# Optimization experiments

Measured on AMD Instinct MI355X. Metric: run time of the kernel, lower is better.

Reference implementation:

```python
import jax, jax.numpy as jnp
import numpy as np

B, S, D, H = 64, 1024, 512, 512

def setup_inputs() -> dict:
    key = jax.random.key(0)
    ks = jax.random.split(key, 10)
    w = 0.04  # ~xavier scale for 512x512
    return {
        "inputs": jax.random.normal(ks[0], (B, S, D), jnp.float32),
        "Wxi": jax.random.normal(ks[1], (D, H), jnp.float32) * w,
        "Whi": jax.random.normal(ks[2], (H, H), jnp.float32) * w,
        "bi": jnp.zeros((H,), jnp.float32),
        "Wxf": jax.random.normal(ks[3], (D, H), jnp.float32) * w,
        "Whf": jax.random.normal(ks[4], (H, H), jnp.float32) * w,
        "bf": jnp.zeros((H,), jnp.float32),
        "Wxo": jax.random.normal(ks[5], (D, H), jnp.float32) * w,
        "Who": jax.random.normal(ks[6], (H, H), jnp.float32) * w,
        "bo": jnp.zeros((H,), jnp.float32),
        "Wxc": jax.random.normal(ks[7], (D, H), jnp.float32) * w,
        "Whc": jax.random.normal(ks[8], (H, H), jnp.float32) * w,
        "bc": jnp.zeros((H,), jnp.float32),
    }

def reference(inputs, Wxi, Whi, bi, Wxf, Whf, bf, Wxo, Who, bo, Wxc, Whc, bc):
    b, s, _ = inputs.shape
    h = Whi.shape[0]
    # Precompute input projections for all timesteps (same math, batched GEMM).
    xi = inputs @ Wxi + bi  # [B,S,H]
    xf = inputs @ Wxf + bf
    xo = inputs @ Wxo + bo
    xc = inputs @ Wxc + bc
    # time-major for scan: [S,B,H]
    xs = tuple(jnp.swapaxes(a, 0, 1) for a in (xi, xf, xo, xc))

    def step(carry, x_t):
        h_t, c_t = carry
        xi_t, xf_t, xo_t, xc_t = x_t
        i = jax.nn.sigmoid(xi_t + h_t @ Whi)
        f = jax.nn.sigmoid(xf_t + h_t @ Whf)
        o = jax.nn.sigmoid(xo_t + h_t @ Who)
        g = jnp.tanh(xc_t + h_t @ Whc)
        c_new = f * c_t + i * g
        h_new = o * jnp.tanh(c_new)
        return (h_new, c_new), h_new

    h0 = jnp.zeros((b, h), inputs.dtype)
    c0 = jnp.zeros((b, h), inputs.dtype)
    (h_fin, c_fin), out = jax.lax.scan(step, (h0, c0), xs)
    outputs = jnp.swapaxes(out, 0, 1)  # [B,S,H]
    h_final = h_fin[None]  # [1,B,H] (num_layers*num_directions=1)
    c_final = c_fin[None]
    return (outputs, h_final, c_final)
```

## Files before the change

kernel.cpp:

```cpp
#include <hip/hip_runtime.h>
#include <hip/hip_bf16.h>

typedef __attribute__((ext_vector_type(8))) short short8;
typedef __attribute__((ext_vector_type(4))) float f32x4;
typedef __attribute__((ext_vector_type(4))) unsigned int u32x4;

#define NB 64
#define NS 1024
#define ND 512
#define NH 512
#define NG 2048
#define M1 65536

#define OFF_A    0L
#define OFF_XG   67108864L
#define OFF_WXT  335544320L
#define OFF_WHT  337641472L
#define OFF_BC   339738624L
#define OFF_HB   339746816L
#define OFF_BAR  339877888L

#define OUT_HF   33554432L
#define OUT_CF   33587200L

#define LDS_STRIDE 264

static __device__ __forceinline__ ushort f2bf(float x) {
  union { float f; unsigned u; } v; v.f = x;
  unsigned r = (v.u + 0x7FFFu + ((v.u >> 16) & 1u)) >> 16;
  return (ushort)r;
}
static __device__ __forceinline__ float bf2f(ushort x) {
  union { unsigned u; float f; } v; v.u = ((unsigned)x) << 16; return v.f;
}
static __device__ __forceinline__ float sigm(float x) {
  return 1.0f / (1.0f + __expf(-x));
}
static __device__ __forceinline__ float tanh_fast(float x) {
  return 2.0f / (1.0f + __expf(-2.0f * x)) - 1.0f;
}

__global__ __launch_bounds__(256) void cvt_in_k(const float* __restrict__ in,
                                                ushort* __restrict__ out) {
  long i = ((long)blockIdx.x * 256 + threadIdx.x) * 8;
  const float4* p = (const float4*)(in + i);
  float4 a = p[0], b = p[1];
  short8 o;
  o[0] = (short)f2bf(a.x); o[1] = (short)f2bf(a.y);
  o[2] = (short)f2bf(a.z); o[3] = (short)f2bf(a.w);
  o[4] = (short)f2bf(b.x); o[5] = (short)f2bf(b.y);
  o[6] = (short)f2bf(b.z); o[7] = (short)f2bf(b.w);
  *(short8*)(out + i) = o;
}

__global__ __launch_bounds__(256) void prep_w_k(
    const float* __restrict__ Wxi, const float* __restrict__ Whi, const float* __restrict__ bi,
    const float* __restrict__ Wxf, const float* __restrict__ Whf, const float* __restrict__ bff,
    const float* __restrict__ Wxo, const float* __restrict__ Who, const float* __restrict__ bo,
    const float* __restrict__ Wxc, const float* __restrict__ Whc, const float* __restrict__ bc,
    ushort* __restrict__ Wxt, ushort* __restrict__ Wht, float* __restrict__ bcat) {
  int t = blockIdx.x * 256 + threadIdx.x;
  int n = t >> 9, k = t & 511;
  int g = n >> 9, col = n & 511;
  const float* wx = (g == 0) ? Wxi : (g == 1) ? Wxf : (g == 2) ? Wxo : Wxc;
  const float* wh = (g == 0) ? Whi : (g == 1) ? Whf : (g == 2) ? Who : Whc;
  Wxt[t] = f2bf(wx[k * 512 + col]);
  Wht[t] = f2bf(wh[k * 512 + col]);
  if (t < 2048) {
    int g2 = t >> 9;
    const float* bp = (g2 == 0) ? bi : (g2 == 1) ? bff : (g2 == 2) ? bo : bc;
    bcat[t] = bp[t & 511];
  }
}

__global__ __launch_bounds__(256) void gemm_x_k(const ushort* __restrict__ A,
                                                const ushort* __restrict__ Bt,
                                                const float* __restrict__ bcat,
                                                ushort* __restrict__ xg) {
  __shared__ ushort As[128 * 40];
  __shared__ ushort Bs[128 * 40];
  const int mbase = blockIdx.x * 128;
  const int nbase = blockIdx.y * 128;
  const int tid = threadIdx.x;
  const int lane = tid & 63, wave = tid >> 6;
  const int l15 = lane & 15, q = lane >> 4;
  const int wm = (wave & 1) * 64, wn = (wave >> 1) * 64;

  f32x4 acc[4][4];
#pragma unroll
  for (int j = 0; j < 4; ++j) {
    float bv = bcat[nbase + wn + j * 16 + l15];
#pragma unroll
    for (int i = 0; i < 4; ++i) acc[i][j] = (f32x4){bv, bv, bv, bv};
  }

  const int sr = tid >> 2;
  const int skk = (tid & 3) * 8;

  for (int kt = 0; kt < 16; ++kt) {
    const int kb = kt * 32;
#pragma unroll
    for (int pass = 0; pass < 2; ++pass) {
      int rr = sr + pass * 64;
      *(short8*)&As[rr * 40 + skk] = *(const short8*)&A[(long)(mbase + rr) * 512 + kb + skk];
      *(short8*)&Bs[rr * 40 + skk] = *(const short8*)&Bt[(long)(nbase + rr) * 512 + kb + skk];
    }
    __syncthreads();
    short8 af[4], bfr[4];
#pragma unroll
    for (int i = 0; i < 4; ++i)
      af[i] = *(const short8*)&As[(wm + i * 16 + l15) * 40 + q * 8];
#pragma unroll
    for (int j = 0; j < 4; ++j)
      bfr[j] = *(const short8*)&Bs[(wn + j * 16 + l15) * 40 + q * 8];
#pragma unroll
    for (int i = 0; i < 4; ++i)
#pragma unroll
      for (int j = 0; j < 4; ++j)
        acc[i][j] = __builtin_amdgcn_mfma_f32_16x16x32_bf16(af[i], bfr[j], acc[i][j], 0, 0, 0);
    __syncthreads();
  }

#pragma unroll
  for (int i = 0; i < 4; ++i) {
#pragma unroll
    for (int r = 0; r < 4; ++r) {
      int m = mbase + wm + i * 16 + q * 4 + r;
      int b = m >> 10, s = m & 1023;
      long rowoff = ((long)(s * 64 + b)) * 2048;
#pragma unroll
      for (int j = 0; j < 4; ++j) {
        int n = nbase + wn + j * 16 + l15;
        xg[rowoff + n] = f2bf(acc[i][j][r]);
      }
    }
  }
}

__global__ __launch_bounds__(256, 1) void lstm_rec_k(const ushort* __restrict__ xg,
                                                     const ushort* __restrict__ Wht,
                                                     float* __restrict__ out,
                                                     unsigned* hb, unsigned* ctrl) {
  const int wg = blockIdx.x;
  const int g = wg & 7, r = wg >> 3;
  const int tid = threadIdx.x;
  const int wave = tid >> 6, lane = tid & 63;
  const int l15 = lane & 15, q = lane >> 4;

  __shared__ unsigned hs[8 * LDS_STRIDE];

  unsigned* fl  = ctrl + g * 32;
  unsigned* hbg = hb + g * 4096;
  const ushort* xgg = xg + (long)g * 8 * 2048;

  short8 bfrag[2][16];
  int gcol[2];
#pragma unroll
  for (int p = 0; p < 2; ++p) {
    int nloc = p * 16 + l15;
    gcol[p] = (nloc >> 3) * 512 + r * 32 + wave * 8 + (nloc & 7);
#pragma unroll
    for (int kt = 0; kt < 16; ++kt)
      bfrag[p][kt] = *(const short8*)&Wht[(long)gcol[p] * 512 + kt * 32 + q * 8];
  }
#pragma unroll
  for (int p = 0; p < 2; ++p)
#pragma unroll
    for (int kt = 0; kt < 16; ++kt)
      asm volatile("" : "+v"(bfrag[p][kt]));

  float xpre[2][4] = {{0.f, 0.f, 0.f, 0.f}, {0.f, 0.f, 0.f, 0.f}};
  if (q < 2) {
#pragma unroll
    for (int p = 0; p < 2; ++p)
#pragma unroll
      for (int rr = 0; rr < 4; ++rr)
        xpre[p][rr] = bf2f(xgg[(long)(q * 4 + rr) * 2048 + gcol[p]]);
  }

  const bool wr = (lane & 8) == 0;
  const bool wrp = wr && ((lane & 1) == 0);
  float c4[4] = {0.f, 0.f, 0.f, 0.f};
  float hsave[4] = {0.f, 0.f, 0.f, 0.f};
  float hpsave[4] = {0.f, 0.f, 0.f, 0.f};

  const int c0 = tid, c1 = tid + 256;
  const int l0 = (c0 >> 6) * LDS_STRIDE + (c0 & 63) * 4;
  const int l1 = (c1 >> 6) * LDS_STRIDE + (c1 & 63) * 4;

  for (int t = 0; t < 1024; ++t) {
    union { unsigned long long u[2]; short8 s8; } afu[16];

    if (t > 0) {
      const unsigned* gb = hbg + (t & 1) * 2048;
      u32x4 va, vb;
      asm volatile(
          "global_load_dwordx4 %0, %2, off sc0 sc1\n\t"
          "global_load_dwordx4 %1, %3, off sc0 sc1"
          : "=&v"(va), "=&v"(vb)
          : "v"(gb + c0 * 4), "v"(gb + c1 * 4)
          : "memory");
      asm volatile("s_waitcnt vmcnt(0)" ::: "memory");
      *(u32x4*)&hs[l0] = va;
      *(u32x4*)&hs[l1] = vb;
      __syncthreads();

      if (l15 < 8) {
        const unsigned* lb = &hs[l15 * LDS_STRIDE + q * 4];
#pragma unroll
        for (int kt = 0; kt < 16; ++kt)
          afu[kt].s8 = *(const short8*)(lb + kt * 16);
      } else {
#pragma unroll
        for (int kt = 0; kt < 16; ++kt) { afu[kt].u[0] = 0ull; afu[kt].u[1] = 0ull; }
      }
    } else {
#pragma unroll
      for (int kt = 0; kt < 16; ++kt) { afu[kt].u[0] = 0ull; afu[kt].u[1] = 0ull; }
    }

    f32x4 acc[2];
#pragma unroll
    for (int p = 0; p < 2; ++p)
#pragma unroll
      for (int rr = 0; rr < 4; ++rr)
        acc[p][rr] = xpre[p][rr];

#pragma unroll
    for (int kt = 0; kt < 16; ++kt) {
      acc[0] = __builtin_amdgcn_mfma_f32_16x16x32_bf16(afu[kt].s8, bfrag[0][kt], acc[0], 0, 0, 0);
      acc[1] = __builtin_amdgcn_mfma_f32_16x16x32_bf16(afu[kt].s8, bfrag[1][kt], acc[1], 0, 0, 0);
    }

    unsigned* hdst = hbg + ((t + 1) & 1) * 2048;
#pragma unroll
    for (int rr = 0; rr < 4; ++rr) {
      float a0 = acc[0][rr], a1 = acc[1][rr];
      float o0 = __shfl_xor(a0, 8);
      float o1 = __shfl_xor(a1, 8);
      float pi = wr ? a0 : o0;
      float pf = wr ? o0 : a0;
      float po = wr ? a1 : o1;
      float pg = wr ? o1 : a1;
      float ig = sigm(pi), fg = sigm(pf), og = sigm(po), gg = tanh_fast(pg);
      float cc = fg * c4[rr] + ig * gg;
      c4[rr] = cc;
      float hn = og * tanh_fast(cc);
      float hnp = __shfl_xor(hn, 1);
      hsave[rr] = hn;
      hpsave[rr] = hnp;
      if (wrp && q < 2 && t < 1023) {
        unsigned pack = (unsigned)f2bf(hn) | ((unsigned)f2bf(hnp) << 16);
        __hip_atomic_store(&hdst[(q * 4 + rr) * 256 + r * 16 + wave * 4 + ((lane & 6) >> 1)],
                           pack, __ATOMIC_RELAXED, __HIP_MEMORY_SCOPE_AGENT);
      }
    }

    if (t < 1023) {
      __syncthreads();
      if (tid == 0)
        __hip_atomic_store(&fl[r], (unsigned)(t + 1), __ATOMIC_RELAXED,
                           __HIP_MEMORY_SCOPE_AGENT);
    }

    if (wrp && q < 2) {
#pragma unroll
      for (int rr = 0; rr < 4; ++rr)
        *(float2*)&out[(long)(g * 8 + q * 4 + rr) * (NS * NH) + (long)t * NH +
                       r * 32 + wave * 8 + (lane & 6)] =
            make_float2(hsave[rr], hpsave[rr]);
    }

    if (t < 1023) {
      long xb2 = ((long)(t + 1) * 64) * 2048;
      if (q < 2) {
#pragma unroll
        for (int p = 0; p < 2; ++p)
#pragma unroll
          for (int rr = 0; rr < 4; ++rr)
            xpre[p][rr] = bf2f(xgg[xb2 + (long)(q * 4 + rr) * 2048 + gcol[p]]);
      }
      if (wave == 0 && lane < 16) {
        unsigned tgt = (unsigned)(t + 1);
        while (__hip_atomic_load(&fl[lane], __ATOMIC_RELAXED,
                                 __HIP_MEMORY_SCOPE_AGENT) < tgt) {}
      }
      __syncthreads();
    }
  }

  if (wr && q < 2) {
    int hcol = r * 32 + wave * 8 + (lane & 7);
#pragma unroll
    for (int rr = 0; rr < 4; ++rr) {
      int b = g * 8 + q * 4 + rr;
      out[OUT_HF + (long)b * 512 + hcol] = hsave[rr];
      out[OUT_CF + (long)b * 512 + hcol] = c4[rr];
    }
  }
}

extern "C" void kernel_launch(void* const* d_in, const int* in_sizes, int n_in,
                              void* d_out, int out_size, void* d_ws, size_t ws_size,
                              hipStream_t stream) {
  const float* inputs = (const float*)d_in[0];
  const float* Wxi = (const float*)d_in[1];
  const float* Whi = (const float*)d_in[2];
  const float* bi  = (const float*)d_in[3];
  const float* Wxf = (const float*)d_in[4];
  const float* Whf = (const float*)d_in[5];
  const float* bff = (const float*)d_in[6];
  const float* Wxo = (const float*)d_in[7];
  const float* Who = (const float*)d_in[8];
  const float* bo  = (const float*)d_in[9];
  const float* Wxc = (const float*)d_in[10];
  const float* Whc = (const float*)d_in[11];
  const float* bc  = (const float*)d_in[12];

  char* ws = (char*)d_ws;
  ushort*  Abf  = (ushort*)(ws + OFF_A);
  ushort*  xgp  = (ushort*)(ws + OFF_XG);
  ushort*  Wxt  = (ushort*)(ws + OFF_WXT);
  ushort*  Whtp = (ushort*)(ws + OFF_WHT);
  float*   bcat = (float*)(ws + OFF_BC);
  unsigned* hb  = (unsigned*)(ws + OFF_HB);
  unsigned* ctrl = (unsigned*)(ws + OFF_BAR);

  hipMemsetAsync(ctrl, 0, 1024, stream);

  cvt_in_k<<<16384, 256, 0, stream>>>(inputs, Abf);
  prep_w_k<<<4096, 256, 0, stream>>>(Wxi, Whi, bi, Wxf, Whf, bff,
                                     Wxo, Who, bo, Wxc, Whc, bc,
                                     Wxt, Whtp, bcat);
  dim3 g1(M1 / 128, NG / 128);
  gemm_x_k<<<g1, 256, 0, stream>>>(Abf, Wxt, bcat, xgp);
  lstm_rec_k<<<128, 256, 0, stream>>>(xgp, Whtp, (float*)d_out, hb, ctrl);
}
```

Measured before the change: 3.375 ms.

## Replace flag barrier with sentinel-tagged triple-buffered hidden-state exchange

Drops the per-group flag counters and the spin-wait barrier in the LSTM recurrence. The hidden-state buffer becomes triple-buffered with a 0xFFFFFFFF sentinel: consumers poll the data itself until no sentinel remains, then reset the slot two steps ahead. This removes a full cross-workgroup round trip (flag store, then poll) from each timestep. In exchange, correctness depends on a bf16 pair never encoding all-ones (a NaN pattern) and on the ordering of the reset stores. The buffer now reuses the converted-input area, so it is memset after the GEMM.

```diff
diff --git a/kernel.cpp b/kernel.cpp
--- a/kernel.cpp
+++ b/kernel.cpp
@@ -17,12 +17,11 @@
 #define OFF_WXT  335544320L
 #define OFF_WHT  337641472L
 #define OFF_BC   339738624L
-#define OFF_HB   339746816L
-#define OFF_BAR  339877888L
 
 #define OUT_HF   33554432L
 #define OUT_CF   33587200L
 
+#define SENT32   0xFFFFFFFFu
 #define LDS_STRIDE 264
 
 static __device__ __forceinline__ ushort f2bf(float x) {
@@ -140,7 +139,7 @@
 __global__ __launch_bounds__(256, 1) void lstm_rec_k(const ushort* __restrict__ xg,
                                                      const ushort* __restrict__ Wht,
                                                      float* __restrict__ out,
-                                                     unsigned* hb, unsigned* ctrl) {
+                                                     unsigned* hb3) {
   const int wg = blockIdx.x;
   const int g = wg & 7, r = wg >> 3;
   const int tid = threadIdx.x;
@@ -149,8 +148,7 @@
 
   __shared__ unsigned hs[8 * LDS_STRIDE];
 
-  unsigned* fl  = ctrl + g * 32;
-  unsigned* hbg = hb + g * 4096;
+  unsigned* hbg = hb3 + g * 6144;
   const ushort* xgg = xg + (long)g * 8 * 2048;
 
   short8 bfrag[2][16];
@@ -187,23 +185,33 @@
   const int c0 = tid, c1 = tid + 256;
   const int l0 = (c0 >> 6) * LDS_STRIDE + (c0 & 63) * 4;
   const int l1 = (c1 >> 6) * LDS_STRIDE + (c1 & 63) * 4;
+  const int woff = q * 1024 + r * 16 + wave * 4 + ((lane & 6) >> 1);
 
   for (int t = 0; t < 1024; ++t) {
     union { unsigned long long u[2]; short8 s8; } afu[16];
 
     if (t > 0) {
-      const unsigned* gb = hbg + (t & 1) * 2048;
+      const unsigned* gb = hbg + (t % 3) * 2048;
       u32x4 va, vb;
-      asm volatile(
-          "global_load_dwordx4 %0, %2, off sc0 sc1\n\t"
-          "global_load_dwordx4 %1, %3, off sc0 sc1"
-          : "=&v"(va), "=&v"(vb)
-          : "v"(gb + c0 * 4), "v"(gb + c1 * 4)
-          : "memory");
-      asm volatile("s_waitcnt vmcnt(0)" ::: "memory");
+      unsigned bad;
+      do {
+        asm volatile(
+            "global_load_dwordx4 %0, %2, off sc0 sc1\n\t"
+            "global_load_dwordx4 %1, %3, off sc0 sc1\n\t"
+            "s_waitcnt vmcnt(0)"
+            : "=&v"(va), "=&v"(vb)
+            : "v"(gb + c0 * 4), "v"(gb + c1 * 4)
+            : "memory");
+        bad = 0;
+#pragma unroll
+        for (int i = 0; i < 4; ++i) {
+          bad |= (unsigned)(va[i] == SENT32);
+          bad |= (unsigned)(vb[i] == SENT32);
+        }
+      } while (bad);
       *(u32x4*)&hs[l0] = va;
       *(u32x4*)&hs[l1] = vb;
-      __syncthreads();
+      asm volatile("s_waitcnt lgkmcnt(0)\n\ts_barrier" ::: "memory");
 
       if (l15 < 8) {
         const unsigned* lb = &hs[l15 * LDS_STRIDE + q * 4];
@@ -214,6 +222,16 @@
 #pragma unroll
         for (int kt = 0; kt < 16; ++kt) { afu[kt].u[0] = 0ull; afu[kt].u[1] = 0ull; }
       }
+
+      if (wrp && q < 2) {
+        unsigned* pp = hbg + ((t + 2) % 3) * 2048 + woff;
+        asm volatile(
+            "global_store_dword %[a], %[s], off sc0 sc1\n\t"
+            "global_store_dword %[a], %[s], off offset:1024 sc0 sc1\n\t"
+            "global_store_dword %[a], %[s], off offset:2048 sc0 sc1\n\t"
+            "global_store_dword %[a], %[s], off offset:3072 sc0 sc1"
+            :: [a]"v"(pp), [s]"v"(SENT32) : "memory");
+      }
     } else {
 #pragma unroll
       for (int kt = 0; kt < 16; ++kt) { afu[kt].u[0] = 0ull; afu[kt].u[1] = 0ull; }
@@ -232,7 +250,7 @@
       acc[1] = __builtin_amdgcn_mfma_f32_16x16x32_bf16(afu[kt].s8, bfrag[1][kt], acc[1], 0, 0, 0);
     }
 
-    unsigned* hdst = hbg + ((t + 1) & 1) * 2048;
+    unsigned packs[4];
 #pragma unroll
     for (int rr = 0; rr < 4; ++rr) {
       float a0 = acc[0][rr], a1 = acc[1][rr];
@@ -249,18 +267,20 @@
       float hnp = __shfl_xor(hn, 1);
       hsave[rr] = hn;
       hpsave[rr] = hnp;
-      if (wrp && q < 2 && t < 1023) {
-        unsigned pack = (unsigned)f2bf(hn) | ((unsigned)f2bf(hnp) << 16);
-        __hip_atomic_store(&hdst[(q * 4 + rr) * 256 + r * 16 + wave * 4 + ((lane & 6) >> 1)],
-                           pack, __ATOMIC_RELAXED, __HIP_MEMORY_SCOPE_AGENT);
-      }
-    }
-
-    if (t < 1023) {
-      __syncthreads();
-      if (tid == 0)
-        __hip_atomic_store(&fl[r], (unsigned)(t + 1), __ATOMIC_RELAXED,
-                           __HIP_MEMORY_SCOPE_AGENT);
+      packs[rr] = (unsigned)f2bf(hn) | ((unsigned)f2bf(hnp) << 16);
+    }
+
+    if (t < 1023 && wrp && q < 2) {
+      unsigned* hd = hbg + ((t + 1) % 3) * 2048 + woff;
+      asm volatile(
+          "s_waitcnt vmcnt(0)\n\t"
+          "global_store_dword %[a], %[d0], off sc0 sc1\n\t"
+          "global_store_dword %[a], %[d1], off offset:1024 sc0 sc1\n\t"
+          "global_store_dword %[a], %[d2], off offset:2048 sc0 sc1\n\t"
+          "global_store_dword %[a], %[d3], off offset:3072 sc0 sc1"
+          :: [a]"v"(hd), [d0]"v"(packs[0]), [d1]"v"(packs[1]),
+             [d2]"v"(packs[2]), [d3]"v"(packs[3])
+          : "memory");
     }
 
     if (wrp && q < 2) {
@@ -280,12 +300,7 @@
           for (int rr = 0; rr < 4; ++rr)
             xpre[p][rr] = bf2f(xgg[xb2 + (long)(q * 4 + rr) * 2048 + gcol[p]]);
       }
-      if (wave == 0 && lane < 16) {
-        unsigned tgt = (unsigned)(t + 1);
-        while (__hip_atomic_load(&fl[lane], __ATOMIC_RELAXED,
-                                 __HIP_MEMORY_SCOPE_AGENT) < tgt) {}
-      }
-      __syncthreads();
+      asm volatile("s_waitcnt lgkmcnt(0)\n\ts_barrier" ::: "memory");
     }
   }
 
@@ -323,10 +338,7 @@
   ushort*  Wxt  = (ushort*)(ws + OFF_WXT);
   ushort*  Whtp = (ushort*)(ws + OFF_WHT);
   float*   bcat = (float*)(ws + OFF_BC);
-  unsigned* hb  = (unsigned*)(ws + OFF_HB);
-  unsigned* ctrl = (unsigned*)(ws + OFF_BAR);
-
-  hipMemsetAsync(ctrl, 0, 1024, stream);
+  unsigned* hb3 = (unsigned*)(ws + OFF_A);
 
   cvt_in_k<<<16384, 256, 0, stream>>>(inputs, Abf);
   prep_w_k<<<4096, 256, 0, stream>>>(Wxi, Whi, bi, Wxf, Whf, bff,
@@ -334,5 +346,6 @@
                                      Wxt, Whtp, bcat);
   dim3 g1(M1 / 128, NG / 128);
   gemm_x_k<<<g1, 256, 0, stream>>>(Abf, Wxt, bcat, xgp);
-  lstm_rec_k<<<128, 256, 0, stream>>>(xgp, Whtp, (float*)d_out, hb, ctrl);
-}
+  hipMemsetAsync(hb3, 0xFF, 196608, stream);
+  lstm_rec_k<<<128, 256, 0, stream>>>(xgp, Whtp, (float*)d_out, hb3);
+}
```

Result: faster. 3.061 ms (-9.3%).
